# Optimization experiments

Measured on AMD Instinct MI355X. Metric: run time of the kernel, lower is better.

The kernel has to match this reference:

```python
import jax, jax.numpy as jnp
import numpy as np

L, B, E, H = 512, 64, 512, 1024

def setup_inputs() -> dict:
    key = jax.random.key(0)
    ks = jax.random.split(key, 10)
    scale = 1.0 / np.sqrt(E + H)  # ~torch Linear init scale
    inp = {
        "x": jax.random.normal(ks[0], (L, B, E), dtype=jnp.float32),
        "c": jnp.zeros((B, H), dtype=jnp.float32),
        "h": jnp.zeros((B, H), dtype=jnp.float32),
    }
    names = ["Wf", "bf", "Wi", "bi", "Wg", "bg", "Wo", "bo"]
    for idx, name in enumerate(names):
        k = ks[idx + 1]
        if name.startswith("W"):
            inp[name] = jax.random.normal(k, (E + H, H), dtype=jnp.float32) * scale
        else:
            inp[name] = jax.random.normal(k, (H,), dtype=jnp.float32) * scale
    return inp


def reference(x, c, h, Wf, bf, Wi, bi, Wg, bg, Wo, bo):
    # Fuse the 4 gate projections into one GEMM: same math since all 4 gates
    # consume the identical concat([x_t, h_{t-1}]) input.
    W = jnp.concatenate([Wf, Wi, Wg, Wo], axis=1)  # (E+H, 4H)
    b = jnp.concatenate([bf, bi, bg, bo])          # (4H,)

    def step(carry, x_t):
        c_prev, h_prev = carry
        xh = jnp.concatenate([x_t, h_prev], axis=-1)       # (B, E+H)
        z = xh @ W + b                                     # (B, 4H)
        f_t, i_t, g_t, o_t = jnp.split(z, 4, axis=-1)
        f_t = jax.nn.sigmoid(f_t)
        i_t = jax.nn.sigmoid(i_t)
        g_t = jnp.tanh(g_t)
        o_t = jax.nn.sigmoid(o_t)
        c_t = c_prev * f_t + i_t * g_t
        h_t = o_t * jnp.tanh(c_t)
        return (c_t, h_t), (c_t, h_t)

    (_, _), (c_full, h_full) = jax.lax.scan(step, (c, h), x)
    return c_full, h_full
```

## Files before the change

### kernel.cpp

```cpp
#include <hip/hip_runtime.h>

typedef unsigned int u32;
typedef unsigned short u16;
using u32x4 = __attribute__((ext_vector_type(4))) u32;
using f16x8 = __attribute__((ext_vector_type(8))) _Float16;
using f32x4 = __attribute__((ext_vector_type(4))) float;

#define LT 512
#define BNB 64
#define ED 512
#define HD 1024
#define OUT_HALF_BYTES ((size_t)LT * BNB * HD * 4)

#define WXP_OFF  ((size_t)0)
#define WHP_OFF  ((size_t)(4u << 20))
#define BIAS_OFF ((size_t)(12u << 20))
#define HSTG_OFF ((size_t)((12u << 20) + (16u << 10)))
#define FLAG_OFF ((size_t)((12u << 20) + (16u << 10) + (512u << 10)))

__device__ __forceinline__ u16 f2h(float f) {
  _Float16 h = (_Float16)f;
  return __builtin_bit_cast(u16, h);
}
__device__ __forceinline__ float h2f(u16 s) {
  return (float)__builtin_bit_cast(_Float16, s);
}
__device__ __forceinline__ u32 pk2(float a, float b) {
  return (u32)f2h(a) | ((u32)f2h(b) << 16);
}
__device__ __forceinline__ void glds16(const void* g, void* l) {
  using GP = const __attribute__((address_space(1))) u32*;
  using SP = __attribute__((address_space(3))) u32*;
  __builtin_amdgcn_global_load_lds((GP)g, (SP)l, 16, 0, 0);
}
__device__ __forceinline__ f32x4 mfma_f16(f16x8 a, f16x8 b, f32x4 c) {
  return __builtin_amdgcn_mfma_f32_16x16x32_f16(a, b, c, 0, 0, 0);
}
__device__ __forceinline__ float sigm(float x) { return 1.0f / (1.0f + __expf(-x)); }
__device__ __forceinline__ float tanh_(float x) { return 2.0f / (1.0f + __expf(-2.0f * x)) - 1.0f; }

__device__ __forceinline__ u32x4 ldg16_cc(const void* p) {
  u32x4 r;
  asm volatile("global_load_dwordx4 %0, %1, off sc0 sc1" : "=v"(r) : "v"(p) : "memory");
  return r;
}
__device__ __forceinline__ u32 ld_flag_cc(const void* p) {
  u32 r;
  asm volatile("global_load_dword %0, %1, off sc0 sc1\n\ts_waitcnt vmcnt(0)"
               : "=v"(r) : "v"(p) : "memory");
  return r;
}
__device__ __forceinline__ void stg_u32_cc(void* p, u32 v) {
  asm volatile("global_store_dword %0, %1, off sc0 sc1" ::"v"(p), "v"(v) : "memory");
}
__device__ __forceinline__ u32 ldg_u16_plain(const void* p) {
  u32 r;
  asm volatile("global_load_ushort %0, %1, off" : "=v"(r) : "v"(p) : "memory");
  return r;
}
__device__ __forceinline__ void waitv0() { asm volatile("s_waitcnt vmcnt(0)" ::: "memory"); }

__device__ __forceinline__ f16x8 unpk(u32x4 lo, u32x4 hi) {
  u32x4 w;
  w[0] = (lo[0] & 0xFFFFu) | (lo[1] << 16);
  w[1] = (lo[2] & 0xFFFFu) | (lo[3] << 16);
  w[2] = (hi[0] & 0xFFFFu) | (hi[1] << 16);
  w[3] = (hi[2] & 0xFFFFu) | (hi[3] << 16);
  return __builtin_bit_cast(f16x8, w);
}


__global__ void pack_wx(const float* __restrict__ Wf, const float* __restrict__ Wi,
                        const float* __restrict__ Wg, const float* __restrict__ Wo,
                        u32x4* __restrict__ dst) {
  const int id = blockIdx.x * 256 + threadIdx.x;
  const int lane = id & 63;
  const int row = id >> 6;
  const int ntile = row >> 7;
  const int rem = row & 127;
  const int kt = rem >> 3;
  const int fn = rem & 7;
  const int np = (ntile << 7) + (fn << 4) + (lane & 15);
  const int g = (np >> 4) & 3;
  const int jfull = ((np >> 6) << 4) + (np & 15);
  const int k0 = (kt << 5) + ((lane >> 4) << 3);
  const float* W = (g == 0) ? Wf : (g == 1) ? Wi : (g == 2) ? Wg : Wo;
  const float* s = W + (size_t)k0 * HD + jfull;
  u16 h[8];
#pragma unroll
  for (int i = 0; i < 8; ++i) h[i] = f2h(s[(size_t)i * HD]);
  u32x4 v;
  v[0] = (u32)h[0] | ((u32)h[1] << 16);
  v[1] = (u32)h[2] | ((u32)h[3] << 16);
  v[2] = (u32)h[4] | ((u32)h[5] << 16);
  v[3] = (u32)h[6] | ((u32)h[7] << 16);
  dst[id] = v;
}

__global__ void pack_wh(const float* __restrict__ Wf, const float* __restrict__ Wi,
                        const float* __restrict__ Wg, const float* __restrict__ Wo,
                        u32x4* __restrict__ dst) {
  const int id = blockIdx.x * 256 + threadIdx.x;
  const int lane = id & 63;
  const int row = id >> 6;
  const int kk = row & 7;
  const int w = (row >> 3) & 3;
  const int nt = (row >> 5) & 7;
  const int cq = row >> 8;
  const int np = (cq << 7) + (nt << 4) + (lane & 15);
  const int g = (np >> 4) & 3;
  const int jfull = ((np >> 6) << 4) + (np & 15);
  const int k = ED + (w << 8) + (kk << 5) + ((lane >> 4) << 3);
  const float* W = (g == 0) ? Wf : (g == 1) ? Wi : (g == 2) ? Wg : Wo;
  const float* s = W + (size_t)k * HD + jfull;
  u16 h[8];
#pragma unroll
  for (int i = 0; i < 8; ++i) h[i] = f2h(s[(size_t)i * HD]);
  u32x4 v;
  v[0] = (u32)h[0] | ((u32)h[1] << 16);
  v[1] = (u32)h[2] | ((u32)h[3] << 16);
  v[2] = (u32)h[4] | ((u32)h[5] << 16);
  v[3] = (u32)h[6] | ((u32)h[7] << 16);
  dst[id] = v;
}

__global__ void pack_bias_flags(const float* __restrict__ bf, const float* __restrict__ bi,
                                const float* __restrict__ bg, const float* __restrict__ bo,
                                float* __restrict__ dst, int* __restrict__ flags) {
  const int id = blockIdx.x * 256 + threadIdx.x;
  const int g = (id >> 4) & 3;
  const int jfull = ((id >> 6) << 4) + (id & 15);
  const float* B = (g == 0) ? bf : (g == 1) ? bi : (g == 2) ? bg : bo;
  dst[id] = B[jfull];
  flags[id] = 0;
}


__global__ __launch_bounds__(256) void zx_gemm(const float* __restrict__ x,
                                               const u32x4* __restrict__ wxp,
                                               const float* __restrict__ biasp,
                                               char* __restrict__ outb) {
  __shared__ u32x4 Ab[512];
  __shared__ u32x4 Bb[512];
  const int bid = blockIdx.x;
  const int ntile = bid & 31;
  const int mtile = bid >> 5;
  const int tid = threadIdx.x;
  const int lane = tid & 63;
  const int wid = tid >> 6;
  const int wm = wid & 1;
  const int wn = wid >> 1;
  const int m0 = mtile << 7;

  const f32x4 fz = {0.f, 0.f, 0.f, 0.f};
  f32x4 acc[4][4];
#pragma unroll
  for (int i = 0; i < 4; ++i)
#pragma unroll
    for (int j = 0; j < 4; ++j) acc[i][j] = fz;

  for (int kt = 0; kt < 16; ++kt) {
#pragma unroll
    for (int r = 0; r < 2; ++r) {
      const int c = tid + (r << 8);
      const int fl = c & 63;
      const int fmg = c >> 6;
      const int row = m0 + (fmg << 4) + (fl & 15);
      const int kc = (kt << 5) + ((fl >> 4) << 3);
      const float* s = x + (size_t)row * ED + kc;
      const float4 p0 = *(const float4*)s;
      const float4 p1 = *(const float4*)(s + 4);
      u32x4 v;
      v[0] = pk2(p0.x, p0.y);
      v[1] = pk2(p0.z, p0.w);
      v[2] = pk2(p1.x, p1.y);
      v[3] = pk2(p1.z, p1.w);
      Ab[c] = v;
    }
    {
      const u32x4* bsrc = wxp + (((size_t)(ntile << 4) + kt) << 9);
#pragma unroll
      for (int r = 0; r < 2; ++r) {
        const int cb = (wid << 6) + (r << 8);
        glds16((const void*)(bsrc + cb + lane), (void*)&Bb[cb]);
      }
    }
    __syncthreads();
    f16x8 afr[4], bfr[4];
#pragma unroll
    for (int f = 0; f < 4; ++f) afr[f] = __builtin_bit_cast(f16x8, Ab[((wm * 4 + f) << 6) + lane]);
#pragma unroll
    for (int f = 0; f < 4; ++f) bfr[f] = __builtin_bit_cast(f16x8, Bb[((wn * 4 + f) << 6) + lane]);
#pragma unroll
    for (int fm = 0; fm < 4; ++fm)
#pragma unroll
      for (int fn = 0; fn < 4; ++fn) acc[fm][fn] = mfma_f16(afr[fm], bfr[fn], acc[fm][fn]);
    __syncthreads();
  }

  char* const cb_ = outb;
  char* const hb_ = outb + OUT_HALF_BYTES;
  const int r0 = (lane >> 4) << 2;
#pragma unroll
  for (int fn = 0; fn < 4; ++fn) {
    const int np = (ntile << 7) + (wn << 6) + (fn << 4) + (lane & 15);
    const float bv = biasp[np];
    const int gg = (np >> 4) & 3;
    const int cg = np >> 6;
    const int jj = np & 15;
    char* const outHalf = (gg < 2) ? cb_ : hb_;
    const size_t coloff = (size_t)(cg << 6) + ((gg & 1) << 5) + (jj << 1);
#pragma unroll
    for (int fm = 0; fm < 4; ++fm) {
#pragma unroll
      for (int r = 0; r < 4; ++r) {
        const int m = m0 + (wm << 6) + (fm << 4) + r0 + r;
        *(u16*)(outHalf + (size_t)m * 4096 + coloff) = f2h(acc[fm][fn][r] + bv);
      }
    }
  }
}


__global__ __launch_bounds__(256, 1) void lstm_rec(const float* __restrict__ c0,
                                                   const float* __restrict__ h0,
                                                   const u32x4* __restrict__ whp, char* outb,
                                                   u32* hstg, int* flags) {
  __shared__ float zb[4][8][16][17];
  const int bid = blockIdx.x;
  const int mslab = bid & 3;
  const int cq = bid >> 2;
  const int tid = threadIdx.x;
  const int lane = tid & 63;
  const int wid = tid >> 6;
  const int b_loc = tid >> 4;
  const int j_loc = tid & 15;
  const int b = (mslab << 4) + b_loc;
  const int col0 = (cq << 5) + j_loc;

  f16x8 wreg[8][8];
#pragma unroll
  for (int nt = 0; nt < 8; ++nt)
#pragma unroll
    for (int kk = 0; kk < 8; ++kk)
      wreg[nt][kk] = __builtin_bit_cast(
          f16x8, whp[((size_t)((cq << 8) + (nt << 5) + (wid << 3) + kk) << 6) + lane]);

  float creg0 = c0[(b << 10) + col0];
  float creg1 = c0[(b << 10) + col0 + 16];
  stg_u32_cc(hstg + (b << 10) + col0, (u32)f2h(h0[(b << 10) + col0]));
  stg_u32_cc(hstg + (b << 10) + col0 + 16, (u32)f2h(h0[(b << 10) + col0 + 16]));

  char* const cb_ = outb;
  char* const hb_ = outb + OUT_HALF_BYTES;

  u32 zx0[4], zx1[4];
  {
    const size_t rowb = ((size_t)b) << 12;
#pragma unroll
    for (int g = 0; g < 4; ++g) {
      const char* half = (g < 2) ? cb_ : hb_;
      zx0[g] = ldg_u16_plain(half + rowb + (cq << 7) + ((g & 1) << 5) + (j_loc << 1));
      zx1[g] = ldg_u16_plain(half + rowb + (cq << 7) + 64 + ((g & 1) << 5) + (j_loc << 1));
    }
  }
  __syncthreads();
  if (tid == 0) stg_u32_cc(flags + (((mslab << 5) + cq) << 2), 1u);

  const u32 aoff = (u32)((((mslab << 4) + (lane & 15)) << 10) + (wid << 8) + ((lane >> 4) << 3));
  const int* const pf = flags + (((mslab << 5) + (lane & 31)) << 2);

  const f32x4 fz = {0.f, 0.f, 0.f, 0.f};
#pragma unroll 1
  for (int t = 0; t < LT; ++t) {
    while ((int)ld_flag_cc(pf) < t + 1) {}

    const u32* ab = hstg + (((u32)t & 1) << 16) + aoff;
    const u32 gtag = (u32)t << 16;
    u32x4 v[16];
    for (;;) {
#pragma unroll
      for (int kk = 0; kk < 8; ++kk) {
        v[2 * kk] = ldg16_cc(ab + (kk << 5));
        v[2 * kk + 1] = ldg16_cc(ab + (kk << 5) + 4);
      }
      waitv0();
      u32 acm = 0;
#pragma unroll
      for (int i = 0; i < 16; ++i)
        acm |= (v[i][0] ^ gtag) | (v[i][1] ^ gtag) | (v[i][2] ^ gtag) | (v[i][3] ^ gtag);
      if (__all(acm < 0x10000u)) break;
    }

    f32x4 acc[8];
#pragma unroll
    for (int nt = 0; nt < 8; ++nt) acc[nt] = fz;
#pragma unroll
    for (int kk = 0; kk < 8; ++kk) {
      const f16x8 av = unpk(v[2 * kk], v[2 * kk + 1]);
#pragma unroll
      for (int nt = 0; nt < 8; ++nt) acc[nt] = mfma_f16(av, wreg[nt][kk], acc[nt]);
    }
    {
      const int rr = (lane >> 4) << 2;
      const int cc = lane & 15;
#pragma unroll
      for (int nt = 0; nt < 8; ++nt)
#pragma unroll
        for (int r = 0; r < 4; ++r) zb[wid][nt][rr + r][cc] = acc[nt][r];
    }
    __syncthreads();

    float hv0, hv1;
    {
      float z[4];
#pragma unroll
      for (int g = 0; g < 4; ++g) {
        float s = h2f((u16)zx0[g]);
#pragma unroll
        for (int w = 0; w < 4; ++w) s += zb[w][g][b_loc][j_loc];
        z[g] = s;
      }
      const float fg = sigm(z[0]), ig = sigm(z[1]), gg = tanh_(z[2]), og = sigm(z[3]);
      creg0 = creg0 * fg + ig * gg;
      hv0 = og * tanh_(creg0);
    }
    {
      float z[4];
#pragma unroll
      for (int g = 0; g < 4; ++g) {
        float s = h2f((u16)zx1[g]);
#pragma unroll
        for (int w = 0; w < 4; ++w) s += zb[w][4 + g][b_loc][j_loc];
        z[g] = s;
      }
      const float fg = sigm(z[0]), ig = sigm(z[1]), gg = tanh_(z[2]), og = sigm(z[3]);
      creg1 = creg1 * fg + ig * gg;
      hv1 = og * tanh_(creg1);
    }

    const u32 ntag = ((u32)(t + 1)) << 16;
    u32* hdst = hstg + ((((u32)(t + 1)) & 1) << 16) + (b << 10) + col0;
    stg_u32_cc(hdst, ntag | (u32)f2h(hv0));
    stg_u32_cc(hdst + 16, ntag | (u32)f2h(hv1));
    __syncthreads();
    if (tid == 0) stg_u32_cc(flags + (((mslab << 5) + cq) << 2), (u32)(t + 2));

    const size_t rowoff = ((size_t)((t << 6) + b)) << 12;
    *(float*)(cb_ + rowoff + ((size_t)col0 << 2)) = creg0;
    *(float*)(cb_ + rowoff + ((size_t)(col0 + 16) << 2)) = creg1;
    *(float*)(hb_ + rowoff + ((size_t)col0 << 2)) = hv0;
    *(float*)(hb_ + rowoff + ((size_t)(col0 + 16) << 2)) = hv1;

    {
      const int tn = (t + 1 < LT) ? t + 1 : t;
      const size_t rown = ((size_t)((tn << 6) + b)) << 12;
#pragma unroll
      for (int g = 0; g < 4; ++g) {
        const char* half = (g < 2) ? cb_ : hb_;
        zx0[g] = ldg_u16_plain(half + rown + (cq << 7) + ((g & 1) << 5) + (j_loc << 1));
        zx1[g] = ldg_u16_plain(half + rown + (cq << 7) + 64 + ((g & 1) << 5) + (j_loc << 1));
      }
    }
  }
}

extern "C" void kernel_launch(void* const* d_in, const int* in_sizes, int n_in, void* d_out,
                              int out_size, void* d_ws, size_t ws_size, hipStream_t stream) {
  const float* x = (const float*)d_in[0];
  const float* c0 = (const float*)d_in[1];
  const float* h0 = (const float*)d_in[2];
  const float* Wf = (const float*)d_in[3];
  const float* bf = (const float*)d_in[4];
  const float* Wi = (const float*)d_in[5];
  const float* bi = (const float*)d_in[6];
  const float* Wg = (const float*)d_in[7];
  const float* bg = (const float*)d_in[8];
  const float* Wo = (const float*)d_in[9];
  const float* bo = (const float*)d_in[10];

  char* ws = (char*)d_ws;
  u32x4* wxp = (u32x4*)(ws + WXP_OFF);
  u32x4* whp = (u32x4*)(ws + WHP_OFF);
  float* bp = (float*)(ws + BIAS_OFF);
  u32* hstg = (u32*)(ws + HSTG_OFF);
  int* flags = (int*)(ws + FLAG_OFF);

  pack_wx<<<1024, 256, 0, stream>>>(Wf, Wi, Wg, Wo, wxp);
  pack_wh<<<2048, 256, 0, stream>>>(Wf, Wi, Wg, Wo, whp);
  pack_bias_flags<<<16, 256, 0, stream>>>(bf, bi, bg, bo, bp, flags);
  zx_gemm<<<8192, 256, 0, stream>>>(x, wxp, bp, (char*)d_out);
  lstm_rec<<<128, 256, 0, stream>>>(c0, h0, whp, (char*)d_out, hstg, flags);
}
```

Before: 2.773 ms.

## Replace tagged h exchange with packed fp16 staging and flag-only sync

The recurrent kernel now stores h as packed fp16 instead of tag-carrying 32-bit words. Each step waits on per-block flags (now padded to separate cache lines) across all lanes, then issues half as many loads with no unpacking or tag validation. The h store and flag release move to the end of the step after the output writes, with an explicit store drain before the barrier. This trades the tag-retry scheme for memory-ordering reliance on waitcnt plus the flag, and adds a store-drain wait on the critical path.

```diff
diff --git a/kernel.cpp b/kernel.cpp
--- a/kernel.cpp
+++ b/kernel.cpp
@@ -50,6 +50,9 @@
                : "=v"(r) : "v"(p) : "memory");
   return r;
 }
+__device__ __forceinline__ void st_u16_cc(void* p, u32 v) {
+  asm volatile("global_store_short %0, %1, off sc0 sc1" ::"v"(p), "v"(v) : "memory");
+}
 __device__ __forceinline__ void stg_u32_cc(void* p, u32 v) {
   asm volatile("global_store_dword %0, %1, off sc0 sc1" ::"v"(p), "v"(v) : "memory");
 }
@@ -59,15 +62,6 @@
   return r;
 }
 __device__ __forceinline__ void waitv0() { asm volatile("s_waitcnt vmcnt(0)" ::: "memory"); }
-
-__device__ __forceinline__ f16x8 unpk(u32x4 lo, u32x4 hi) {
-  u32x4 w;
-  w[0] = (lo[0] & 0xFFFFu) | (lo[1] << 16);
-  w[1] = (lo[2] & 0xFFFFu) | (lo[3] << 16);
-  w[2] = (hi[0] & 0xFFFFu) | (hi[1] << 16);
-  w[3] = (hi[2] & 0xFFFFu) | (hi[3] << 16);
-  return __builtin_bit_cast(f16x8, w);
-}
 
 
 __global__ void pack_wx(const float* __restrict__ Wf, const float* __restrict__ Wi,
@@ -128,10 +122,12 @@
                                 const float* __restrict__ bg, const float* __restrict__ bo,
                                 float* __restrict__ dst, int* __restrict__ flags) {
   const int id = blockIdx.x * 256 + threadIdx.x;
-  const int g = (id >> 4) & 3;
-  const int jfull = ((id >> 6) << 4) + (id & 15);
-  const float* B = (g == 0) ? bf : (g == 1) ? bi : (g == 2) ? bg : bo;
-  dst[id] = B[jfull];
+  if (id < 4096) {
+    const int g = (id >> 4) & 3;
+    const int jfull = ((id >> 6) << 4) + (id & 15);
+    const float* B = (g == 0) ? bf : (g == 1) ? bi : (g == 2) ? bg : bo;
+    dst[id] = B[jfull];
+  }
   flags[id] = 0;
 }
 
@@ -225,7 +221,7 @@
 __global__ __launch_bounds__(256, 1) void lstm_rec(const float* __restrict__ c0,
                                                    const float* __restrict__ h0,
                                                    const u32x4* __restrict__ whp, char* outb,
-                                                   u32* hstg, int* flags) {
+                                                   u16* hstage, int* flags) {
   __shared__ float zb[4][8][16][17];
   const int bid = blockIdx.x;
   const int mslab = bid & 3;
@@ -248,8 +244,6 @@
 
   float creg0 = c0[(b << 10) + col0];
   float creg1 = c0[(b << 10) + col0 + 16];
-  stg_u32_cc(hstg + (b << 10) + col0, (u32)f2h(h0[(b << 10) + col0]));
-  stg_u32_cc(hstg + (b << 10) + col0 + 16, (u32)f2h(h0[(b << 10) + col0 + 16]));
 
   char* const cb_ = outb;
   char* const hb_ = outb + OUT_HALF_BYTES;
@@ -264,40 +258,36 @@
       zx1[g] = ldg_u16_plain(half + rowb + (cq << 7) + 64 + ((g & 1) << 5) + (j_loc << 1));
     }
   }
+  st_u16_cc(hstage + (b << 10) + col0, (u32)f2h(h0[(b << 10) + col0]));
+  st_u16_cc(hstage + (b << 10) + col0 + 16, (u32)f2h(h0[(b << 10) + col0 + 16]));
+  waitv0();
   __syncthreads();
-  if (tid == 0) stg_u32_cc(flags + (((mslab << 5) + cq) << 2), 1u);
+  if (tid == 0) stg_u32_cc(flags + (((mslab << 5) + cq) << 5), 1u);
 
   const u32 aoff = (u32)((((mslab << 4) + (lane & 15)) << 10) + (wid << 8) + ((lane >> 4) << 3));
-  const int* const pf = flags + (((mslab << 5) + (lane & 31)) << 2);
+  const int* const pf = flags + (((mslab << 5) + (lane & 31)) << 5);
 
   const f32x4 fz = {0.f, 0.f, 0.f, 0.f};
 #pragma unroll 1
   for (int t = 0; t < LT; ++t) {
-    while ((int)ld_flag_cc(pf) < t + 1) {}
-
-    const u32* ab = hstg + (((u32)t & 1) << 16) + aoff;
-    const u32 gtag = (u32)t << 16;
-    u32x4 v[16];
-    for (;;) {
-#pragma unroll
-      for (int kk = 0; kk < 8; ++kk) {
-        v[2 * kk] = ldg16_cc(ab + (kk << 5));
-        v[2 * kk + 1] = ldg16_cc(ab + (kk << 5) + 4);
-      }
-      waitv0();
-      u32 acm = 0;
-#pragma unroll
-      for (int i = 0; i < 16; ++i)
-        acm |= (v[i][0] ^ gtag) | (v[i][1] ^ gtag) | (v[i][2] ^ gtag) | (v[i][3] ^ gtag);
-      if (__all(acm < 0x10000u)) break;
-    }
+    u32 fl;
+    do {
+      fl = (u32)ld_flag_cc(pf);
+    } while (!__all((int)(fl >= (u32)(t + 1))));
+
+    const u16* ab = hstage + (((u32)t & 1) << 16) + aoff;
+    u32x4 v[8];
+#pragma unroll
+    for (int kk = 0; kk < 8; ++kk) v[kk] = ldg16_cc(ab + (kk << 5));
+    waitv0();
+    __builtin_amdgcn_sched_barrier(0);
 
     f32x4 acc[8];
 #pragma unroll
     for (int nt = 0; nt < 8; ++nt) acc[nt] = fz;
 #pragma unroll
     for (int kk = 0; kk < 8; ++kk) {
-      const f16x8 av = unpk(v[2 * kk], v[2 * kk + 1]);
+      const f16x8 av = __builtin_bit_cast(f16x8, v[kk]);
 #pragma unroll
       for (int nt = 0; nt < 8; ++nt) acc[nt] = mfma_f16(av, wreg[nt][kk], acc[nt]);
     }
@@ -338,20 +328,12 @@
       creg1 = creg1 * fg + ig * gg;
       hv1 = og * tanh_(creg1);
     }
-
-    const u32 ntag = ((u32)(t + 1)) << 16;
-    u32* hdst = hstg + ((((u32)(t + 1)) & 1) << 16) + (b << 10) + col0;
-    stg_u32_cc(hdst, ntag | (u32)f2h(hv0));
-    stg_u32_cc(hdst + 16, ntag | (u32)f2h(hv1));
-    __syncthreads();
-    if (tid == 0) stg_u32_cc(flags + (((mslab << 5) + cq) << 2), (u32)(t + 2));
 
     const size_t rowoff = ((size_t)((t << 6) + b)) << 12;
     *(float*)(cb_ + rowoff + ((size_t)col0 << 2)) = creg0;
     *(float*)(cb_ + rowoff + ((size_t)(col0 + 16) << 2)) = creg1;
     *(float*)(hb_ + rowoff + ((size_t)col0 << 2)) = hv0;
     *(float*)(hb_ + rowoff + ((size_t)(col0 + 16) << 2)) = hv1;
-
     {
       const int tn = (t + 1 < LT) ? t + 1 : t;
       const size_t rown = ((size_t)((tn << 6) + b)) << 12;
@@ -362,6 +344,13 @@
         zx1[g] = ldg_u16_plain(half + rown + (cq << 7) + 64 + ((g & 1) << 5) + (j_loc << 1));
       }
     }
+
+    u16* hdst = hstage + ((((u32)(t + 1)) & 1) << 16) + (b << 10) + col0;
+    st_u16_cc(hdst, (u32)f2h(hv0));
+    st_u16_cc(hdst + 16, (u32)f2h(hv1));
+    waitv0();
+    __syncthreads();
+    if (tid == 0) stg_u32_cc(flags + (((mslab << 5) + cq) << 5), (u32)(t + 2));
   }
 }
 
@@ -383,12 +372,12 @@
   u32x4* wxp = (u32x4*)(ws + WXP_OFF);
   u32x4* whp = (u32x4*)(ws + WHP_OFF);
   float* bp = (float*)(ws + BIAS_OFF);
-  u32* hstg = (u32*)(ws + HSTG_OFF);
+  u16* hstage = (u16*)(ws + HSTG_OFF);
   int* flags = (int*)(ws + FLAG_OFF);
 
   pack_wx<<<1024, 256, 0, stream>>>(Wf, Wi, Wg, Wo, wxp);
   pack_wh<<<2048, 256, 0, stream>>>(Wf, Wi, Wg, Wo, whp);
-  pack_bias_flags<<<16, 256, 0, stream>>>(bf, bi, bg, bo, bp, flags);
+  pack_bias_flags<<<32, 256, 0, stream>>>(bf, bi, bg, bo, bp, flags);
   zx_gemm<<<8192, 256, 0, stream>>>(x, wxp, bp, (char*)d_out);
-  lstm_rec<<<128, 256, 0, stream>>>(c0, h0, whp, (char*)d_out, hstg, flags);
-}
+  lstm_rec<<<128, 256, 0, stream>>>(c0, h0, whp, (char*)d_out, hstage, flags);
+}
```

Result: faster. 2.401 ms (-13.4%).
